# Kernel optimization log

Measured on AMD Instinct MI355X. Metric: run time of the kernel, lower is better.

The kernel has to match this reference:

```python
import jax, jax.numpy as jnp
import numpy as np

B, S, D = 4, 2048, 1024
M, CH = 16, 256  # experts, chunk size (4096 // 16)


def make_preds(m):
    # Watts-Strogatz ring lattice (n=m, k=4), edges oriented min->max => DAG.
    preds = []
    for v in range(m):
        p = set()
        if v >= 1:
            p.add(v - 1)
        if v >= 2:
            p.add(v - 2)
        if v == m - 2:
            p.add(0)          # wrap edge {m-2, 0}
        if v == m - 1:
            p.update((0, 1))  # wrap edges {m-1, 0}, {m-1, 1}
        preds.append(sorted(p))
    return preds

PREDS = make_preds(M)


def layernorm(x, g, b, eps=1e-5):
    mu = x.mean(-1, keepdims=True)
    var = ((x - mu) ** 2).mean(-1, keepdims=True)
    return (x - mu) * jax.lax.rsqrt(var + eps) * g + b


def setup_inputs() -> dict:
    key = jax.random.key(0)
    ks = jax.random.split(key, 8)
    sc_in = 1.0 / np.sqrt(D)
    sc_ch = 1.0 / np.sqrt(CH)
    return {
        "x": jax.random.normal(ks[0], (B, S, D), jnp.float32),
        "norm_g": jnp.ones((D,), jnp.float32),
        "norm_b": jnp.zeros((D,), jnp.float32),
        "fc1_w": jax.random.normal(ks[1], (M, CH, D), jnp.float32) * sc_in,
        "fc1_b": jax.random.normal(ks[2], (M, CH), jnp.float32) * 0.02,
        "ln_g": jnp.ones((M, CH), jnp.float32),
        "ln_b": jnp.zeros((M, CH), jnp.float32),
        "fc2_w": jax.random.normal(ks[3], (M, D, CH), jnp.float32) * sc_ch,
        "fc2_bias": jax.random.normal(ks[4], (D,), jnp.float32) * 0.02,
        "router_w": jax.random.normal(ks[5], (M, 4, D), jnp.float32) * sc_in,
        "router_b": jax.random.normal(ks[6], (M, 4), jnp.float32) * 0.02,
    }


def reference(x, norm_g, norm_b, fc1_w, fc1_b, ln_g, ln_b, fc2_w, fc2_bias,
              router_w, router_b):
    m = fc1_w.shape[0]
    x_norm = layernorm(x, norm_g, norm_b)
    outs = []
    for v in range(m):  # 0..m-1 is a topological order (all edges low->high)
        pv = PREDS[v]
        if pv:
            npred = len(pv)
            logits = jnp.einsum('bsd,pd->bsp', x_norm, router_w[v, :npred]) \
                     + router_b[v, :npred]
            w = jax.nn.sigmoid(logits)                                # [B,S,P]
            pred_stack = jnp.stack([outs[u] for u in pv], axis=-1)    # [B,S,D,P]
            node_in = jnp.einsum('bsdp,bsp->bsd', pred_stack, w)
        else:
            node_in = x_norm
        h = jax.nn.gelu(jnp.einsum('bsd,cd->bsc', node_in, fc1_w[v]) + fc1_b[v],
                        approximate=False)
        h = layernorm(h, ln_g[v], ln_b[v])
        outs.append(jnp.einsum('bsc,dc->bsd', h, fc2_w[v]))  # fc2 bias zeroed per-node
    combined = outs[m - 1] + fc2_bias  # node m-1 is the unique terminal node
    return x + combined  # use_residual=True
```

## Files before the change

### kernel.cpp

```cpp
#include <hip/hip_runtime.h>
#include <hip/hip_bf16.h>

typedef _Float16 f16;
typedef _Float16 f16x8 __attribute__((ext_vector_type(8)));
typedef float f32x4 __attribute__((ext_vector_type(4)));

#define TOKS 8192
#define DDIM 1024
#define CHDIM 256

__device__ __constant__ int c_OFF[16]  = {0,0,1,3,5,7,9,11,13,15,17,19,21,23,25,28};
__device__ __constant__ int c_NP[16]   = {0,1,2,2,2,2,2,2,2,2,2,2,2,2,3,4};
__device__ __constant__ int c_RROW[32] = {4, 8,9, 12,13, 16,17, 20,21, 24,25, 28,29, 32,33, 36,37, 40,41, 44,45, 48,49, 52,53, 56,57,58, 60,61,62,63};

__device__ __forceinline__ f16x8 sp8(f16 w){
  f16x8 r;
  #pragma unroll
  for (int j=0;j<8;++j) r[j]=w;
  return r;
}

__global__ __launch_bounds__(256) void k_prep(const float* __restrict__ x, const float* __restrict__ g,
                                              const float* __restrict__ b, f16* __restrict__ xn,
                                              const float* __restrict__ rw, const float* __restrict__ rb,
                                              float* __restrict__ wsig,
                                              const float* __restrict__ w1, const float* __restrict__ w2,
                                              f16* __restrict__ w1p, f16* __restrict__ w2p){
  const int blk = blockIdx.x, tid = threadIdx.x;
  if (blk < 2048){
    const int lane = tid & 63, wv = tid >> 6;
    const int tk = blk*4 + wv;
    const float* xp = x + (size_t)tk*DDIM + lane*16;
    float xv[16];
    #pragma unroll
    for (int j=0;j<16;j+=4){ const float4 f=*(const float4*)(xp+j); xv[j]=f.x; xv[j+1]=f.y; xv[j+2]=f.z; xv[j+3]=f.w; }
    float s=0.f, q=0.f;
    #pragma unroll
    for (int j=0;j<16;++j){ s += xv[j]; q += xv[j]*xv[j]; }
    #pragma unroll
    for (int m=1;m<64;m<<=1){ s += __shfl_xor(s,m); q += __shfl_xor(q,m); }
    const float mu = s*(1.f/DDIM);
    const float rs = rsqrtf(q*(1.f/DDIM) - mu*mu + 1e-5f);
    #pragma unroll
    for (int j=0;j<16;j+=4){
      const float4 gg=*(const float4*)(g + lane*16 + j);
      const float4 bb=*(const float4*)(b + lane*16 + j);
      xv[j]   = (xv[j]  -mu)*rs*gg.x + bb.x;
      xv[j+1] = (xv[j+1]-mu)*rs*gg.y + bb.y;
      xv[j+2] = (xv[j+2]-mu)*rs*gg.z + bb.z;
      xv[j+3] = (xv[j+3]-mu)*rs*gg.w + bb.w;
    }
    f16x8 o0, o1;
    #pragma unroll
    for (int j=0;j<8;++j){ o0[j] = (f16)xv[j]; o1[j] = (f16)xv[8+j]; }
    *(f16x8*)(xn + (size_t)tk*DDIM + lane*16)     = o0;
    *(f16x8*)(xn + (size_t)tk*DDIM + lane*16 + 8) = o1;
    for (int e=0;e<32;++e){
      const int row = c_RROW[e];
      const float* rp = rw + (size_t)row*DDIM + lane*16;
      float d = 0.f;
      #pragma unroll
      for (int j=0;j<16;j+=4){
        const float4 f=*(const float4*)(rp+j);
        d += xv[j]*f.x + xv[j+1]*f.y + xv[j+2]*f.z + xv[j+3]*f.w;
      }
      #pragma unroll
      for (int m=1;m<64;m<<=1) d += __shfl_xor(d,m);
      if (lane==0) wsig[tk*32 + e] = 1.f/(1.f + expf(-(d + rb[row])));
    }
  } else if (blk < 4096){
    const int c = (blk-2048)*256 + tid;
    const int l15 = c & 15, g4 = (c>>4)&3, ic = (c>>6)&31, wvv = (c>>11)&15, v = c>>15;
    const float* s = w1 + (size_t)v*262144 + (size_t)(wvv*16 + l15)*1024 + ic*32 + g4*8;
    const float4 a = *(const float4*)s, b4 = *(const float4*)(s+4);
    f16x8 o;
    o[0]=(f16)a.x; o[1]=(f16)a.y; o[2]=(f16)a.z; o[3]=(f16)a.w;
    o[4]=(f16)b4.x; o[5]=(f16)b4.y; o[6]=(f16)b4.z; o[7]=(f16)b4.w;
    *(f16x8*)(w1p + (size_t)c*8) = o;
  } else {
    const int c = (blk-4096)*256 + tid;
    const int l15 = c & 15, g4 = (c>>4)&3, nf = (c>>6)&3, ks = (c>>8)&7, wvv = (c>>11)&15, v = c>>15;
    const float* s = w2 + (size_t)v*262144 + (size_t)(wvv*64 + nf*16 + l15)*256 + ks*32 + g4*8;
    const float4 a = *(const float4*)s, b4 = *(const float4*)(s+4);
    f16x8 o;
    o[0]=(f16)a.x; o[1]=(f16)a.y; o[2]=(f16)a.z; o[3]=(f16)a.w;
    o[4]=(f16)b4.x; o[5]=(f16)b4.y; o[6]=(f16)b4.z; o[7]=(f16)b4.w;
    *(f16x8*)(w2p + (size_t)c*8) = o;
  }
}

__global__ __launch_bounds__(1024,4) void k_moe(
    const f16* __restrict__ xn, const f16* __restrict__ w1p, const f16* __restrict__ w2p,
    const float* __restrict__ fc1b, const float* __restrict__ lng, const float* __restrict__ lnb,
    const float* __restrict__ f2bias, const float* __restrict__ wsigG,
    const float* __restrict__ x, float* __restrict__ out, f16* __restrict__ gouts)
{
  __shared__ f16 wsg[32][32];
  __shared__ __align__(16) f16 Pbuf0[32*1032];
  __shared__ __align__(16) f16 Pbuf1[32*1032];
  __shared__ __align__(16) f16 hln[32*264];
  __shared__ float part[32][17][2];
  __shared__ float musq[32][2];

  const int tid = threadIdx.x;
  const int lane = tid & 63, wv = tid >> 6;
  const int l15 = lane & 15, g4 = (lane >> 4) & 3;
  const int blk = blockIdx.x, tok0 = blk * 32;
  const f32x4 fzero = {0.f,0.f,0.f,0.f};

  wsg[tid>>5][tid&31] = (f16)wsigG[tok0*32 + tid];

  f16* Pp = Pbuf0;
  f16* Pc = Pbuf1;

  for (int v=0; v<16; ++v){
    const f16* bp1 = w1p + (size_t)(v*16 + wv)*16384 + lane*8;
    f16x8 pb[12];
    #pragma unroll
    for (int j=0;j<12;++j) pb[j] = *(const f16x8*)(bp1 + j*512);

    if (v == 0){
      #pragma unroll
      for (int p=0;p<4;++p){
        const int c = tid + p*1024, t = c>>7, c8 = (c&127)*8;
        *(f16x8*)&Pc[t*1032 + c8] = *(const f16x8*)(xn + (size_t)(tok0+t)*DDIM + c8);
      }
    } else {
      const int np = c_NP[v], off = c_OFF[v];
      const int ech = off + np - 1, ev2 = off + np - 2, nex = np - 2;
      #pragma unroll
      for (int p=0;p<4;++p){
        const int c = tid + p*1024, t = c>>7, c8 = (c&127)*8;
        const f16x8 pv = *(const f16x8*)&Pp[t*1032 + c8];
        if (v <= 2)
          *(f16x8*)(gouts + (size_t)(v-1)*TOKS*DDIM + (size_t)(tok0+t)*DDIM + c8) = pv;
        f16x8 acc = sp8(wsg[t][ech]) * pv;
        if (np >= 2){
          const f16x8 p2 = *(const f16x8*)&Pc[t*1032 + c8];
          acc += sp8(wsg[t][ev2]) * p2;
        }
        if (nex >= 1){
          const f16x8 e0 = *(const f16x8*)(gouts + (size_t)(tok0+t)*DDIM + c8);
          acc += sp8(wsg[t][off]) * e0;
        }
        if (nex >= 2){
          const f16x8 e1 = *(const f16x8*)(gouts + (size_t)TOKS*DDIM + (size_t)(tok0+t)*DDIM + c8);
          acc += sp8(wsg[t][off+1]) * e1;
        }
        *(f16x8*)&Pc[t*1032 + c8] = acc;
      }
    }
    __syncthreads();

    f32x4 acc1[2] = {fzero, fzero};
    #pragma unroll
    for (int ic=0; ic<32; ++ic){
      const f16x8 b = pb[ic%12];
      if (ic < 20) pb[ic%12] = *(const f16x8*)(bp1 + (ic+12)*512);
      const f16x8 a0 = *(const f16x8*)&Pc[l15*1032      + ic*32 + g4*8];
      const f16x8 a1 = *(const f16x8*)&Pc[(16+l15)*1032 + ic*32 + g4*8];
      acc1[0] = __builtin_amdgcn_mfma_f32_16x16x32_f16(a0, b, acc1[0], 0,0,0);
      acc1[1] = __builtin_amdgcn_mfma_f32_16x16x32_f16(a1, b, acc1[1], 0,0,0);
    }

    const f16* bp2 = w2p + (size_t)(v*16 + wv)*16384 + lane*8;
    f16x8 pc2[12];
    #pragma unroll
    for (int j=0;j<12;++j) pc2[j] = *(const f16x8*)(bp2 + j*512);

    const int c1 = wv*16 + l15;
    const float fb = fc1b[v*CHDIM + c1];
    const float lg = lng[v*CHDIM + c1], lb = lnb[v*CHDIM + c1];
    #pragma unroll
    for (int mf=0;mf<2;++mf)
      #pragma unroll
      for (int r=0;r<4;++r){
        const float h = acc1[mf][r] + fb;
        acc1[mf][r] = 0.5f*h*(1.f + erff(h*0.70710678118654752f));
      }
    #pragma unroll
    for (int mf=0;mf<2;++mf)
      #pragma unroll
      for (int r=0;r<4;++r){
        float s = acc1[mf][r], q = s*s;
        #pragma unroll
        for (int m=1;m<16;m<<=1){ s += __shfl_xor(s,m); q += __shfl_xor(q,m); }
        if (l15==0){ const int t = mf*16 + g4*4 + r; part[t][wv][0]=s; part[t][wv][1]=q; }
      }
    __syncthreads();
    if (tid < 32){
      float s=0.f, q=0.f;
      #pragma unroll
      for (int w=0;w<16;++w){ s += part[tid][w][0]; q += part[tid][w][1]; }
      const float mu = s*(1.f/CHDIM);
      musq[tid][0] = mu;
      musq[tid][1] = rsqrtf(q*(1.f/CHDIM) - mu*mu + 1e-5f);
    }
    __syncthreads();
    #pragma unroll
    for (int mf=0;mf<2;++mf)
      #pragma unroll
      for (int r=0;r<4;++r){
        const int t = mf*16 + g4*4 + r;
        hln[t*264 + c1] = (f16)((acc1[mf][r]-musq[t][0])*musq[t][1]*lg + lb);
      }
    __syncthreads();

    f32x4 acc2[2][4];
    #pragma unroll
    for (int mf=0;mf<2;++mf)
      #pragma unroll
      for (int nf=0;nf<4;++nf) acc2[mf][nf] = fzero;
    f16x8 a0h, a1h;
    #pragma unroll
    for (int cki=0; cki<32; ++cki){
      const int ks = cki>>2, nf = cki&3;
      if (nf == 0){
        a0h = *(const f16x8*)&hln[l15*264      + ks*32 + g4*8];
        a1h = *(const f16x8*)&hln[(16+l15)*264 + ks*32 + g4*8];
      }
      const f16x8 b = pc2[cki%12];
      if (cki < 20) pc2[cki%12] = *(const f16x8*)(bp2 + (cki+12)*512);
      acc2[0][nf] = __builtin_amdgcn_mfma_f32_16x16x32_f16(a0h, b, acc2[0][nf], 0,0,0);
      acc2[1][nf] = __builtin_amdgcn_mfma_f32_16x16x32_f16(a1h, b, acc2[1][nf], 0,0,0);
    }
    #pragma unroll
    for (int mf=0;mf<2;++mf)
      #pragma unroll
      for (int nf=0;nf<4;++nf){
        const int c2 = wv*64 + nf*16 + l15;
        const float fb2 = (v==15) ? f2bias[c2] : 0.f;
        #pragma unroll
        for (int r=0;r<4;++r){
          const int t = mf*16 + g4*4 + r;
          Pc[t*1032 + c2] = (f16)(acc2[mf][nf][r] + fb2);
        }
      }
    __syncthreads();

    if (v == 15){
      #pragma unroll
      for (int p=0;p<4;++p){
        const int c = tid + p*1024, t = c>>7, c8 = (c&127)*8;
        const f16x8 val = *(const f16x8*)&Pc[t*1032 + c8];
        const size_t gi = (size_t)(tok0+t)*DDIM + c8;
        const float4 x0 = *(const float4*)(x+gi), x1 = *(const float4*)(x+gi+4);
        float4 o0, o1;
        o0.x = x0.x + (float)val[0]; o0.y = x0.y + (float)val[1];
        o0.z = x0.z + (float)val[2]; o0.w = x0.w + (float)val[3];
        o1.x = x1.x + (float)val[4]; o1.y = x1.y + (float)val[5];
        o1.z = x1.z + (float)val[6]; o1.w = x1.w + (float)val[7];
        *(float4*)(out+gi) = o0; *(float4*)(out+gi+4) = o1;
      }
    }
    f16* tmp = Pp; Pp = Pc; Pc = tmp;
  }
}

extern "C" void kernel_launch(void* const* d_in, const int* in_sizes, int n_in,
                              void* d_out, int out_size, void* d_ws, size_t ws_size,
                              hipStream_t stream) {
  (void)in_sizes; (void)n_in; (void)out_size; (void)ws_size;
  const float* x   = (const float*)d_in[0];
  const float* ng  = (const float*)d_in[1];
  const float* nb_ = (const float*)d_in[2];
  const float* w1  = (const float*)d_in[3];
  const float* f1b = (const float*)d_in[4];
  const float* lg  = (const float*)d_in[5];
  const float* lb  = (const float*)d_in[6];
  const float* w2  = (const float*)d_in[7];
  const float* f2b = (const float*)d_in[8];
  const float* rw  = (const float*)d_in[9];
  const float* rb  = (const float*)d_in[10];
  float* out = (float*)d_out;

  char* ws = (char*)d_ws;
  f16*  xnh  = (f16*)(ws);
  f16*  w1p  = (f16*)(ws + 16777216);
  f16*  w2p  = (f16*)(ws + 16777216 + 8388608);
  float* wsg = (float*)(ws + 16777216 + 8388608 + 8388608);
  f16*  gouts= (f16*)(ws + 16777216 + 8388608 + 8388608 + 1048576);

  k_prep<<<6144, 256, 0, stream>>>(x, ng, nb_, xnh, rw, rb, wsg, w1, w2, w1p, w2p);
  k_moe<<<256, 1024, 0, stream>>>(xnh, w1p, w2p, f1b, lg, lb, f2b, wsg, x, out, gouts);
}
```

Before: 394.8 us.

## Stagger weight k-order per block, repad LDS rows, raise MFMA priority, tanh-GELU

Each block now walks the K dimension of both GEMMs in a rotated order offset by its block index, so concurrent blocks fetch different weight slices and contend less on the same cache lines and channels. The P buffer row pitch changes from 1032 to 1048 halves to shift LDS bank mapping. MFMA loops are wrapped in s_setprio raises. The exact erf GELU is replaced with the tanh approximation written via a fast exp, which lowers ALU cost but departs slightly from the reference's exact GELU and may affect accuracy tolerance.

Result: slower. 692.3 us (+75.4%).

```diff
diff --git a/kernel.cpp b/kernel.cpp
--- a/kernel.cpp
+++ b/kernel.cpp
@@ -8,6 +8,7 @@
 #define TOKS 8192
 #define DDIM 1024
 #define CHDIM 256
+#define PROW 1048
 
 __device__ __constant__ int c_OFF[16]  = {0,0,1,3,5,7,9,11,13,15,17,19,21,23,25,28};
 __device__ __constant__ int c_NP[16]   = {0,1,2,2,2,2,2,2,2,2,2,2,2,2,3,4};
@@ -96,8 +97,8 @@
     const float* __restrict__ x, float* __restrict__ out, f16* __restrict__ gouts)
 {
   __shared__ f16 wsg[32][32];
-  __shared__ __align__(16) f16 Pbuf0[32*1032];
-  __shared__ __align__(16) f16 Pbuf1[32*1032];
+  __shared__ __align__(16) f16 Pbuf0[32*PROW];
+  __shared__ __align__(16) f16 Pbuf1[32*PROW];
   __shared__ __align__(16) f16 hln[32*264];
   __shared__ float part[32][17][2];
   __shared__ float musq[32][2];
@@ -117,13 +118,13 @@
     const f16* bp1 = w1p + (size_t)(v*16 + wv)*16384 + lane*8;
     f16x8 pb[12];
     #pragma unroll
-    for (int j=0;j<12;++j) pb[j] = *(const f16x8*)(bp1 + j*512);
+    for (int j=0;j<12;++j) pb[j] = *(const f16x8*)(bp1 + ((j+blk)&31)*512);
 
     if (v == 0){
       #pragma unroll
       for (int p=0;p<4;++p){
         const int c = tid + p*1024, t = c>>7, c8 = (c&127)*8;
-        *(f16x8*)&Pc[t*1032 + c8] = *(const f16x8*)(xn + (size_t)(tok0+t)*DDIM + c8);
+        *(f16x8*)&Pc[t*PROW + c8] = *(const f16x8*)(xn + (size_t)(tok0+t)*DDIM + c8);
       }
     } else {
       const int np = c_NP[v], off = c_OFF[v];
@@ -131,12 +132,12 @@
       #pragma unroll
       for (int p=0;p<4;++p){
         const int c = tid + p*1024, t = c>>7, c8 = (c&127)*8;
-        const f16x8 pv = *(const f16x8*)&Pp[t*1032 + c8];
+        const f16x8 pv = *(const f16x8*)&Pp[t*PROW + c8];
         if (v <= 2)
           *(f16x8*)(gouts + (size_t)(v-1)*TOKS*DDIM + (size_t)(tok0+t)*DDIM + c8) = pv;
         f16x8 acc = sp8(wsg[t][ech]) * pv;
         if (np >= 2){
-          const f16x8 p2 = *(const f16x8*)&Pc[t*1032 + c8];
+          const f16x8 p2 = *(const f16x8*)&Pc[t*PROW + c8];
           acc += sp8(wsg[t][ev2]) * p2;
         }
         if (nex >= 1){
@@ -147,26 +148,32 @@
           const f16x8 e1 = *(const f16x8*)(gouts + (size_t)TOKS*DDIM + (size_t)(tok0+t)*DDIM + c8);
           acc += sp8(wsg[t][off+1]) * e1;
         }
-        *(f16x8*)&Pc[t*1032 + c8] = acc;
+        *(f16x8*)&Pc[t*PROW + c8] = acc;
       }
     }
     __syncthreads();
 
     f32x4 acc1[2] = {fzero, fzero};
+    __builtin_amdgcn_s_setprio(1);
     #pragma unroll
     for (int ic=0; ic<32; ++ic){
+      const int icr = (ic + blk) & 31;
       const f16x8 b = pb[ic%12];
-      if (ic < 20) pb[ic%12] = *(const f16x8*)(bp1 + (ic+12)*512);
-      const f16x8 a0 = *(const f16x8*)&Pc[l15*1032      + ic*32 + g4*8];
-      const f16x8 a1 = *(const f16x8*)&Pc[(16+l15)*1032 + ic*32 + g4*8];
+      if (ic < 20) pb[ic%12] = *(const f16x8*)(bp1 + ((ic+12+blk)&31)*512);
+      const f16x8 a0 = *(const f16x8*)&Pc[l15*PROW      + icr*32 + g4*8];
+      const f16x8 a1 = *(const f16x8*)&Pc[(16+l15)*PROW + icr*32 + g4*8];
       acc1[0] = __builtin_amdgcn_mfma_f32_16x16x32_f16(a0, b, acc1[0], 0,0,0);
       acc1[1] = __builtin_amdgcn_mfma_f32_16x16x32_f16(a1, b, acc1[1], 0,0,0);
     }
+    __builtin_amdgcn_s_setprio(0);
 
     const f16* bp2 = w2p + (size_t)(v*16 + wv)*16384 + lane*8;
     f16x8 pc2[12];
     #pragma unroll
-    for (int j=0;j<12;++j) pc2[j] = *(const f16x8*)(bp2 + j*512);
+    for (int j=0;j<12;++j){
+      const int ks = j>>2, nf = j&3, ksr = (ks+blk)&7;
+      pc2[j] = *(const f16x8*)(bp2 + (ksr*4+nf)*512);
+    }
 
     const int c1 = wv*16 + l15;
     const float fb = fc1b[v*CHDIM + c1];
@@ -176,7 +183,7 @@
       #pragma unroll
       for (int r=0;r<4;++r){
         const float h = acc1[mf][r] + fb;
-        acc1[mf][r] = 0.5f*h*(1.f + erff(h*0.70710678118654752f));
+        acc1[mf][r] = h / (1.f + __expf(-1.5957691216057308f*(h + 0.044715f*h*h*h)));
       }
     #pragma unroll
     for (int mf=0;mf<2;++mf)
@@ -212,18 +219,23 @@
       #pragma unroll
       for (int nf=0;nf<4;++nf) acc2[mf][nf] = fzero;
     f16x8 a0h, a1h;
+    __builtin_amdgcn_s_setprio(1);
     #pragma unroll
     for (int cki=0; cki<32; ++cki){
-      const int ks = cki>>2, nf = cki&3;
+      const int ks = cki>>2, nf = cki&3, ksr = (ks+blk)&7;
       if (nf == 0){
-        a0h = *(const f16x8*)&hln[l15*264      + ks*32 + g4*8];
-        a1h = *(const f16x8*)&hln[(16+l15)*264 + ks*32 + g4*8];
+        a0h = *(const f16x8*)&hln[l15*264      + ksr*32 + g4*8];
+        a1h = *(const f16x8*)&hln[(16+l15)*264 + ksr*32 + g4*8];
       }
       const f16x8 b = pc2[cki%12];
-      if (cki < 20) pc2[cki%12] = *(const f16x8*)(bp2 + (cki+12)*512);
+      if (cki < 20){
+        const int ks2 = (cki+12)>>2, nf2 = (cki+12)&3, ksr2 = (ks2+blk)&7;
+        pc2[cki%12] = *(const f16x8*)(bp2 + (ksr2*4+nf2)*512);
+      }
       acc2[0][nf] = __builtin_amdgcn_mfma_f32_16x16x32_f16(a0h, b, acc2[0][nf], 0,0,0);
       acc2[1][nf] = __builtin_amdgcn_mfma_f32_16x16x32_f16(a1h, b, acc2[1][nf], 0,0,0);
     }
+    __builtin_amdgcn_s_setprio(0);
     #pragma unroll
     for (int mf=0;mf<2;++mf)
       #pragma unroll
@@ -233,7 +245,7 @@
         #pragma unroll
         for (int r=0;r<4;++r){
           const int t = mf*16 + g4*4 + r;
-          Pc[t*1032 + c2] = (f16)(acc2[mf][nf][r] + fb2);
+          Pc[t*PROW + c2] = (f16)(acc2[mf][nf][r] + fb2);
         }
       }
     __syncthreads();
@@ -242,7 +254,7 @@
       #pragma unroll
       for (int p=0;p<4;++p){
         const int c = tid + p*1024, t = c>>7, c8 = (c&127)*8;
-        const f16x8 val = *(const f16x8*)&Pc[t*1032 + c8];
+        const f16x8 val = *(const f16x8*)&Pc[t*PROW + c8];
         const size_t gi = (size_t)(tok0+t)*DDIM + c8;
         const float4 x0 = *(const float4*)(x+gi), x1 = *(const float4*)(x+gi+4);
         float4 o0, o1;
```
